# Performance work log

Measured on AMD Instinct MI355X. Metric: run time of the kernel, lower is better.

Reference implementation:

```python
import jax, jax.numpy as jnp
import numpy as np

B, S, D = 2, 2048, 2048
H, KVH = 32, 8
HD = D // H            # 64
G = H // KVH           # 4 kv groups
SCALE = 1.0 / np.sqrt(HD)


def setup_inputs() -> dict:
    key = jax.random.key(0)
    k1, k2, k3, k4, k5 = jax.random.split(key, 5)
    hidden_states = jax.random.normal(k1, (B, S, D), dtype=jnp.float32)
    Wq = jax.random.normal(k2, (D, H * HD), dtype=jnp.float32) * 0.02
    Wk = jax.random.normal(k3, (D, KVH * HD), dtype=jnp.float32) * 0.02
    Wv = jax.random.normal(k4, (D, KVH * HD), dtype=jnp.float32) * 0.02
    Wo = jax.random.normal(k5, (H * HD, D), dtype=jnp.float32) * 0.02
    return {"hidden_states": hidden_states, "Wq": Wq, "Wk": Wk, "Wv": Wv, "Wo": Wo}


def reference(hidden_states, Wq, Wk, Wv, Wo):
    B_, S_, _ = hidden_states.shape
    q = (hidden_states @ Wq).reshape(B_, S_, H, HD).transpose(0, 2, 1, 3)      # [B,H,S,HD]
    k = (hidden_states @ Wk).reshape(B_, S_, KVH, HD).transpose(0, 2, 1, 3)    # [B,KVH,S,HD]
    v = (hidden_states @ Wv).reshape(B_, S_, KVH, HD).transpose(0, 2, 1, 3)
    # repeat_interleave over head dim: kv head g serves q heads [g*G, (g+1)*G)
    k = jnp.repeat(k, G, axis=1)  # [B,H,S,HD]
    v = jnp.repeat(v, G, axis=1)
    scores = jnp.einsum('bhqd,bhkd->bhqk', q, k) * SCALE
    probs = jax.nn.softmax(scores.astype(jnp.float32), axis=-1).astype(q.dtype)
    # dropout is identity in eval mode
    out = jnp.einsum('bhqk,bhkd->bhqd', probs, v)             # [B,H,S,HD]
    out = out.transpose(0, 2, 1, 3).reshape(B_, S_, H * HD)   # [B,S,D]
    return out @ Wo
```

## Files before the change

### kernel.cpp

```cpp
#include <hip/hip_runtime.h>
#include <hip/hip_bf16.h>

typedef unsigned short u16;
typedef __attribute__((ext_vector_type(8))) short short8;
typedef __attribute__((ext_vector_type(4))) float f32x4;
typedef __attribute__((ext_vector_type(16))) float f32x16;
typedef __attribute__((ext_vector_type(4))) unsigned short u16x4;
typedef __attribute__((ext_vector_type(4))) int int4v;

#define S_LEN 2048
#define NH 32
#define NKV 8
#define QSCALE 0.18033688011112042f
#define PSHIFT 14.0f

__device__ __forceinline__ float fexp2(float x) { return __builtin_amdgcn_exp2f(x); }

__device__ __forceinline__ u16 f2bf(float f) {
  unsigned int u = __builtin_bit_cast(unsigned int, f);
  u += 0x7fffu + ((u >> 16) & 1u);
  return (u16)(u >> 16);
}

__device__ __forceinline__ unsigned int pk2bf(float a, float b) {
  float2 t; t.x = a; t.y = b;
  __hip_bfloat162 h = __float22bfloat162_rn(t);
  unsigned int r;
  __builtin_memcpy(&r, &h, 4);
  return r;
}

__device__ __forceinline__ void async16(const void* g, void* l) {
  __builtin_amdgcn_global_load_lds(
      (__attribute__((address_space(1))) void*)g,
      (__attribute__((address_space(3))) void*)l, 16, 0, 0);
}

__device__ __forceinline__ short8 mk_pf(unsigned a, unsigned b, unsigned c, unsigned d) {
  int4v t; t.x = (int)a; t.y = (int)b; t.z = (int)c; t.w = (int)d;
  return __builtin_bit_cast(short8, t);
}

__global__ __launch_bounds__(256) void prep_kernel(const float* __restrict__ X,
                                                   const float* __restrict__ Wq,
                                                   const float* __restrict__ Wk,
                                                   const float* __restrict__ Wv,
                                                   const float* __restrict__ Wo,
                                                   u16* __restrict__ Xb,
                                                   u16* __restrict__ Wqt,
                                                   u16* __restrict__ Wkt,
                                                   u16* __restrict__ Wvt,
                                                   u16* __restrict__ Wot) {
  __shared__ float tile[32][33];
  int bx = blockIdx.x, tid = threadIdx.x;
  if (bx < 8192) {
    int idx = bx * 256 + tid;
    float4 v = ((const float4*)X)[idx];
    u16x4 o;
    o.x = f2bf(v.x); o.y = f2bf(v.y); o.z = f2bf(v.z); o.w = f2bf(v.w);
    *(u16x4*)&Xb[(size_t)idx * 4] = o;
    return;
  }
  const float* in; u16* out; int N, bi;
  if (bx < 12288)      { bi = bx - 8192;  in = Wq; out = Wqt; N = 2048; }
  else if (bx < 13312) { bi = bx - 12288; in = Wk; out = Wkt; N = 512; }
  else if (bx < 14336) { bi = bx - 13312; in = Wv; out = Wvt; N = 512; }
  else                 { bi = bx - 14336; in = Wo; out = Wot; N = 2048; }
  const int K = 2048;
  int nbx = N >> 5;
  int n0 = (bi % nbx) * 32, k0 = (bi / nbx) * 32;
  int tx = tid & 31, ty = tid >> 5;
#pragma unroll
  for (int i = 0; i < 32; i += 8)
    tile[ty + i][tx] = in[(size_t)(k0 + ty + i) * N + n0 + tx];
  __syncthreads();
#pragma unroll
  for (int i = 0; i < 32; i += 8)
    out[(size_t)(n0 + ty + i) * K + k0 + tx] = f2bf(tile[tx][ty + i]);
}

__global__ __launch_bounds__(256) void gemm_qkv(const u16* __restrict__ A,
                                                const u16* __restrict__ Wqt,
                                                const u16* __restrict__ Wkvt,
                                                u16* __restrict__ Qb,
                                                u16* __restrict__ KVb) {
  __shared__ u16 lds_a[128 * 32];
  __shared__ u16 lds_b[128 * 32];
  int tid = threadIdx.x, bx = blockIdx.x;
  int mode, bm, bn;
  const u16* Bt;
  if (bx < 512) { mode = 0; bm = bx >> 4; bn = bx & 15; Bt = Wqt; }
  else          { mode = 1; int b2 = bx - 512; bm = b2 >> 3; bn = b2 & 7; Bt = Wkvt; }
  const int K = 2048;
  int w = tid >> 6, lane = tid & 63, qd = lane >> 4, ln = lane & 15;
  int wm = w >> 1, wn = w & 1;
  const f32x4 z4 = {0.f, 0.f, 0.f, 0.f};
  f32x4 acc[4][4];
#pragma unroll
  for (int i = 0; i < 4; ++i)
#pragma unroll
    for (int j = 0; j < 4; ++j) acc[i][j] = z4;

  const u16* Ab = A + (size_t)bm * 128 * K;
  const u16* Bb = Bt + (size_t)bn * 128 * K;
  int row0 = tid >> 2, c0 = tid & 3;
  int g0 = c0 ^ (row0 & 3) ^ ((row0 >> 2) & 3);
  int s1 = tid + 256, row1 = s1 >> 2, c1 = s1 & 3;
  int g1 = c1 ^ (row1 & 3) ^ ((row1 >> 2) & 3);
  int pat = (ln & 3) ^ ((ln >> 2) & 3);
  int goff = (qd ^ pat) * 8;

  for (int kt = 0; kt < K; kt += 32) {
    async16(Ab + (size_t)row0 * K + kt + g0 * 8, &lds_a[tid * 8]);
    async16(Ab + (size_t)row1 * K + kt + g1 * 8, &lds_a[2048 + tid * 8]);
    async16(Bb + (size_t)row0 * K + kt + g0 * 8, &lds_b[tid * 8]);
    async16(Bb + (size_t)row1 * K + kt + g1 * 8, &lds_b[2048 + tid * 8]);
    __syncthreads();
    short8 af[4], bf[4];
#pragma unroll
    for (int i = 0; i < 4; ++i)
      af[i] = *(const short8*)&lds_a[(wm * 64 + i * 16 + ln) * 32 + goff];
#pragma unroll
    for (int j = 0; j < 4; ++j)
      bf[j] = *(const short8*)&lds_b[(wn * 64 + j * 16 + ln) * 32 + goff];
#pragma unroll
    for (int i = 0; i < 4; ++i)
#pragma unroll
      for (int j = 0; j < 4; ++j)
        acc[i][j] = __builtin_amdgcn_mfma_f32_16x16x32_bf16(af[i], bf[j], acc[i][j], 0, 0, 0);
    __syncthreads();
  }

#pragma unroll
  for (int i = 0; i < 4; ++i)
#pragma unroll
    for (int r = 0; r < 4; ++r) {
      int m = bm * 128 + wm * 64 + i * 16 + qd * 4 + r;
      int b = m >> 11, s = m & 2047;
#pragma unroll
      for (int j = 0; j < 4; ++j) {
        int n = bn * 128 + wn * 64 + j * 16 + ln;
        float v = acc[i][j][r];
        int hh = n >> 6, hd = n & 63;
        if (mode == 0) {
          Qb[(((size_t)(b * NH + hh)) * S_LEN + s) * 64 + hd] = f2bf(v * QSCALE);
        } else {
          if (hh < 8)
            KVb[(((size_t)(b * NKV + hh)) * S_LEN + s) * 64 + hd] = f2bf(v);
          else
            KVb[2097152 + (((size_t)(b * NKV + (hh - 8))) * 64 + hd) * S_LEN + s] = f2bf(v);
        }
      }
    }
}

__global__ __launch_bounds__(256) void gemm_out(const u16* __restrict__ A,
                                                const u16* __restrict__ Bt,
                                                float* __restrict__ outp) {
  __shared__ u16 lds_a[128 * 32];
  __shared__ u16 lds_b[128 * 32];
  const int K = 2048, N = 2048;
  int tid = threadIdx.x;
  int bm = blockIdx.x >> 4, bn = blockIdx.x & 15;
  int w = tid >> 6, lane = tid & 63, qd = lane >> 4, ln = lane & 15;
  int wm = w >> 1, wn = w & 1;
  const f32x4 z4 = {0.f, 0.f, 0.f, 0.f};
  f32x4 acc[4][4];
#pragma unroll
  for (int i = 0; i < 4; ++i)
#pragma unroll
    for (int j = 0; j < 4; ++j) acc[i][j] = z4;

  const u16* Ab = A + (size_t)bm * 128 * K;
  const u16* Bb = Bt + (size_t)bn * 128 * K;
  int row0 = tid >> 2, c0 = tid & 3;
  int g0 = c0 ^ (row0 & 3) ^ ((row0 >> 2) & 3);
  int s1 = tid + 256, row1 = s1 >> 2, c1 = s1 & 3;
  int g1 = c1 ^ (row1 & 3) ^ ((row1 >> 2) & 3);
  int pat = (ln & 3) ^ ((ln >> 2) & 3);
  int goff = (qd ^ pat) * 8;

  for (int kt = 0; kt < K; kt += 32) {
    async16(Ab + (size_t)row0 * K + kt + g0 * 8, &lds_a[tid * 8]);
    async16(Ab + (size_t)row1 * K + kt + g1 * 8, &lds_a[2048 + tid * 8]);
    async16(Bb + (size_t)row0 * K + kt + g0 * 8, &lds_b[tid * 8]);
    async16(Bb + (size_t)row1 * K + kt + g1 * 8, &lds_b[2048 + tid * 8]);
    __syncthreads();
    short8 af[4], bf[4];
#pragma unroll
    for (int i = 0; i < 4; ++i)
      af[i] = *(const short8*)&lds_a[(wm * 64 + i * 16 + ln) * 32 + goff];
#pragma unroll
    for (int j = 0; j < 4; ++j)
      bf[j] = *(const short8*)&lds_b[(wn * 64 + j * 16 + ln) * 32 + goff];
#pragma unroll
    for (int i = 0; i < 4; ++i)
#pragma unroll
      for (int j = 0; j < 4; ++j)
        acc[i][j] = __builtin_amdgcn_mfma_f32_16x16x32_bf16(af[i], bf[j], acc[i][j], 0, 0, 0);
    __syncthreads();
  }

#pragma unroll
  for (int i = 0; i < 4; ++i)
#pragma unroll
    for (int r = 0; r < 4; ++r) {
      int m = bm * 128 + wm * 64 + i * 16 + qd * 4 + r;
#pragma unroll
      for (int j = 0; j < 4; ++j) {
        int n = bn * 128 + wn * 64 + j * 16 + ln;
        outp[(size_t)m * N + n] = acc[i][j][r];
      }
    }
}

__global__ __launch_bounds__(256) void attn_kernel(const u16* __restrict__ Q,
                                                   const u16* __restrict__ K,
                                                   const u16* __restrict__ VT,
                                                   u16* __restrict__ Ao) {
  __shared__ u16 lds_k[2][4096];
  __shared__ u16 lds_v[2][4096];
  int tid = threadIdx.x;
  int w = tid >> 6, lane = tid & 63;
  int l31 = lane & 31, l5 = lane >> 5;
  int qt = blockIdx.x & 15, bh = blockIdx.x >> 4;
  int b = bh >> 5, h = bh & 31, g = h >> 2;
  const u16* gQ = Q + ((size_t)bh * S_LEN + qt * 128) * 64;
  const u16* gK = K + (size_t)(b * NKV + g) * S_LEN * 64;
  const u16* gV = VT + (size_t)(b * NKV + g) * 64 * S_LEN;

  int p7 = l31 & 7;

  int s0 = tid, r0 = s0 >> 3, c0 = s0 & 7, gg0 = c0 ^ (r0 & 7);
  int s1 = tid + 256, r1 = s1 >> 3, c1 = s1 & 7, gg1 = c1 ^ (r1 & 7);

  u16* qstage = &lds_k[0][0];
#pragma unroll
  for (int k = 0; k < 4; ++k) {
    int s = tid + k * 256;
    int q = s >> 3, c = s & 7, gg = c ^ (q & 7);
    async16(gQ + (size_t)q * 64 + gg * 8, &qstage[s * 8]);
  }
  __syncthreads();
  short8 qf[4];
  int qrow = w * 32 + l31;
#pragma unroll
  for (int ks = 0; ks < 4; ++ks)
    qf[ks] = *(const short8*)&qstage[qrow * 64 + ((ks * 2 + l5) ^ p7) * 8];
  __syncthreads();

  async16(gK + (size_t)r0 * 64 + gg0 * 8, &lds_k[0][s0 * 8]);
  async16(gK + (size_t)r1 * 64 + gg1 * 8, &lds_k[0][s1 * 8]);
  async16(gV + (size_t)r0 * S_LEN + gg0 * 8, &lds_v[0][s0 * 8]);
  async16(gV + (size_t)r1 * S_LEN + gg1 * 8, &lds_v[0][s1 * 8]);

  const f32x16 psh16 = {-PSHIFT, -PSHIFT, -PSHIFT, -PSHIFT, -PSHIFT, -PSHIFT,
                        -PSHIFT, -PSHIFT, -PSHIFT, -PSHIFT, -PSHIFT, -PSHIFT,
                        -PSHIFT, -PSHIFT, -PSHIFT, -PSHIFT};
  f32x16 accO[2];
#pragma unroll
  for (int hb = 0; hb < 2; ++hb)
#pragma unroll
    for (int t = 0; t < 16; ++t) accO[hb][t] = 0.f;
  float li = 0.f;

  for (int c = 0; c < 32; ++c) {
    int cur = c & 1;
    if (c < 31) {
      int nb = cur ^ 1, cn = c + 1;
      async16(gK + (size_t)(cn * 64 + r0) * 64 + gg0 * 8, &lds_k[nb][s0 * 8]);
      async16(gK + (size_t)(cn * 64 + r1) * 64 + gg1 * 8, &lds_k[nb][s1 * 8]);
      async16(gV + (size_t)r0 * S_LEN + cn * 64 + gg0 * 8, &lds_v[nb][s0 * 8]);
      async16(gV + (size_t)r1 * S_LEN + cn * 64 + gg1 * 8, &lds_v[nb][s1 * 8]);
    }
    const u16* kb = lds_k[cur];
    const u16* vb = lds_v[cur];

#pragma unroll
    for (int kblk = 0; kblk < 2; ++kblk) {
      f32x16 sc = psh16;
      __builtin_amdgcn_s_setprio(1);
#pragma unroll
      for (int ks = 0; ks < 4; ++ks) {
        short8 kf = *(const short8*)&kb[(kblk * 32 + l31) * 64 + ((ks * 2 + l5) ^ p7) * 8];
        sc = __builtin_amdgcn_mfma_f32_32x32x16_bf16(kf, qf[ks], sc, 0, 0, 0);
      }
      __builtin_amdgcn_s_setprio(0);

      float p[16];
#pragma unroll
      for (int t = 0; t < 16; ++t) p[t] = fexp2(sc[t]);
#pragma unroll
      for (int t = 0; t < 16; t += 4) li += (p[t] + p[t + 1]) + (p[t + 2] + p[t + 3]);
      unsigned W[8];
#pragma unroll
      for (int t = 0; t < 8; ++t) W[t] = pk2bf(p[2 * t], p[2 * t + 1]);
      auto ra = __builtin_amdgcn_permlane32_swap((int)W[0], (int)W[2], false, false);
      auto rb = __builtin_amdgcn_permlane32_swap((int)W[1], (int)W[3], false, false);
      auto rc = __builtin_amdgcn_permlane32_swap((int)W[4], (int)W[6], false, false);
      auto rd = __builtin_amdgcn_permlane32_swap((int)W[5], (int)W[7], false, false);
      short8 pf0 = mk_pf((unsigned)ra[0], (unsigned)rb[0], (unsigned)ra[1], (unsigned)rb[1]);
      short8 pf1 = mk_pf((unsigned)rc[0], (unsigned)rd[0], (unsigned)rc[1], (unsigned)rd[1]);

      __builtin_amdgcn_s_setprio(1);
#pragma unroll
      for (int hb = 0; hb < 2; ++hb) {
        short8 vf = *(const short8*)&vb[(hb * 32 + l31) * 64 + ((kblk * 4 + l5) ^ p7) * 8];
        accO[hb] = __builtin_amdgcn_mfma_f32_32x32x16_bf16(vf, pf0, accO[hb], 0, 0, 0);
      }
#pragma unroll
      for (int hb = 0; hb < 2; ++hb) {
        short8 vf = *(const short8*)&vb[(hb * 32 + l31) * 64 + ((kblk * 4 + 2 + l5) ^ p7) * 8];
        accO[hb] = __builtin_amdgcn_mfma_f32_32x32x16_bf16(vf, pf1, accO[hb], 0, 0, 0);
      }
      __builtin_amdgcn_s_setprio(0);
    }
    __syncthreads();
  }

  float l = li + __shfl_xor(li, 32);
  float inv = 1.f / l;
  int q = qt * 128 + w * 32 + l31;
  size_t base = ((size_t)b * S_LEN + q) * 2048 + h * 64;
#pragma unroll
  for (int hb = 0; hb < 2; ++hb)
#pragma unroll
    for (int rq = 0; rq < 4; ++rq) {
      u16x4 o;
#pragma unroll
      for (int rr = 0; rr < 4; ++rr) o[rr] = f2bf(accO[hb][rq * 4 + rr] * inv);
      *(u16x4*)&Ao[base + hb * 32 + rq * 8 + l5 * 4] = o;
    }
}

extern "C" void kernel_launch(void* const* d_in, const int* in_sizes, int n_in,
                              void* d_out, int out_size, void* d_ws, size_t ws_size,
                              hipStream_t stream) {
  const float* X  = (const float*)d_in[0];
  const float* Wq = (const float*)d_in[1];
  const float* Wk = (const float*)d_in[2];
  const float* Wv = (const float*)d_in[3];
  const float* Wo = (const float*)d_in[4];
  char* ws = (char*)d_ws;
  u16* Xb  = (u16*)(ws);
  u16* Wqt = (u16*)(ws + 16777216);
  u16* Wkt = (u16*)(ws + 25165824);
  u16* Wvt = (u16*)(ws + 27262976);
  u16* Wot = (u16*)(ws + 29360128);
  u16* Qb  = (u16*)(ws + 37748736);
  u16* Kb  = (u16*)(ws + 54525952);
  u16* VTb = (u16*)(ws + 58720256);
  u16* Ab  = (u16*)(ws + 62914560);
  float* out = (float*)d_out;

  prep_kernel<<<18432, 256, 0, stream>>>(X, Wq, Wk, Wv, Wo, Xb, Wqt, Wkt, Wvt, Wot);
  gemm_qkv<<<768, 256, 0, stream>>>(Xb, Wqt, Wkt, Qb, Kb);
  attn_kernel<<<1024, 256, 0, stream>>>(Qb, Kb, VTb, Ab);
  gemm_out<<<512, 256, 0, stream>>>(Ab, Wot, out);
}
```

Baseline: 331.5 us.

## Double-buffer LDS tiles in QKV and output GEMMs with MFMA priority boost

Both projection GEMMs now use two LDS buffers per operand and prefetch the next K-slice with async copies while MFMAs run on the current slice. This is meant to hide global-load latency, which the old single-buffer loop exposed every iteration. s_setprio is raised around the MFMA block to favour matrix issue. LDS use doubles to 32KB per block, which may lower occupancy, and correctness depends on __syncthreads (which waits on vmcnt) ordering the async copies.

```diff
diff --git a/kernel.cpp b/kernel.cpp
--- a/kernel.cpp
+++ b/kernel.cpp
@@ -84,8 +84,7 @@
                                                 const u16* __restrict__ Wkvt,
                                                 u16* __restrict__ Qb,
                                                 u16* __restrict__ KVb) {
-  __shared__ u16 lds_a[128 * 32];
-  __shared__ u16 lds_b[128 * 32];
+  __shared__ u16 la0[4096], la1[4096], lb0[4096], lb1[4096];
   int tid = threadIdx.x, bx = blockIdx.x;
   int mode, bm, bn;
   const u16* Bt;
@@ -94,12 +93,11 @@
   const int K = 2048;
   int w = tid >> 6, lane = tid & 63, qd = lane >> 4, ln = lane & 15;
   int wm = w >> 1, wn = w & 1;
-  const f32x4 z4 = {0.f, 0.f, 0.f, 0.f};
   f32x4 acc[4][4];
 #pragma unroll
   for (int i = 0; i < 4; ++i)
 #pragma unroll
-    for (int j = 0; j < 4; ++j) acc[i][j] = z4;
+    for (int j = 0; j < 4; ++j) acc[i][j] = {0.f, 0.f, 0.f, 0.f};
 
   const u16* Ab = A + (size_t)bm * 128 * K;
   const u16* Bb = Bt + (size_t)bn * 128 * K;
@@ -109,27 +107,45 @@
   int g1 = c1 ^ (row1 & 3) ^ ((row1 >> 2) & 3);
   int pat = (ln & 3) ^ ((ln >> 2) & 3);
   int goff = (qd ^ pat) * 8;
-
-  for (int kt = 0; kt < K; kt += 32) {
-    async16(Ab + (size_t)row0 * K + kt + g0 * 8, &lds_a[tid * 8]);
-    async16(Ab + (size_t)row1 * K + kt + g1 * 8, &lds_a[2048 + tid * 8]);
-    async16(Bb + (size_t)row0 * K + kt + g0 * 8, &lds_b[tid * 8]);
-    async16(Bb + (size_t)row1 * K + kt + g1 * 8, &lds_b[2048 + tid * 8]);
-    __syncthreads();
-    short8 af[4], bf[4];
-#pragma unroll
-    for (int i = 0; i < 4; ++i)
-      af[i] = *(const short8*)&lds_a[(wm * 64 + i * 16 + ln) * 32 + goff];
-#pragma unroll
-    for (int j = 0; j < 4; ++j)
-      bf[j] = *(const short8*)&lds_b[(wn * 64 + j * 16 + ln) * 32 + goff];
-#pragma unroll
-    for (int i = 0; i < 4; ++i)
-#pragma unroll
-      for (int j = 0; j < 4; ++j)
-        acc[i][j] = __builtin_amdgcn_mfma_f32_16x16x32_bf16(af[i], bf[j], acc[i][j], 0, 0, 0);
-    __syncthreads();
-  }
+  const u16* pa0 = Ab + (size_t)row0 * K + g0 * 8;
+  const u16* pa1 = Ab + (size_t)row1 * K + g1 * 8;
+  const u16* pb0 = Bb + (size_t)row0 * K + g0 * 8;
+  const u16* pb1 = Bb + (size_t)row1 * K + g1 * 8;
+
+#define QKV_STAGE(LA, LB, OFS)                      \
+  async16(pa0 + (OFS), &LA[tid * 8]);               \
+  async16(pa1 + (OFS), &LA[2048 + tid * 8]);        \
+  async16(pb0 + (OFS), &LB[tid * 8]);               \
+  async16(pb1 + (OFS), &LB[2048 + tid * 8]);
+
+#define QKV_COMPUTE(LA, LB)                                                        \
+  {                                                                                \
+    short8 af[4], bf[4];                                                           \
+    _Pragma("unroll") for (int i = 0; i < 4; ++i)                                  \
+        af[i] = *(const short8*)&LA[(wm * 64 + i * 16 + ln) * 32 + goff];          \
+    _Pragma("unroll") for (int j = 0; j < 4; ++j)                                  \
+        bf[j] = *(const short8*)&LB[(wn * 64 + j * 16 + ln) * 32 + goff];          \
+    __builtin_amdgcn_s_setprio(1);                                                 \
+    _Pragma("unroll") for (int i = 0; i < 4; ++i)                                  \
+      _Pragma("unroll") for (int j = 0; j < 4; ++j)                                \
+        acc[i][j] =                                                                \
+            __builtin_amdgcn_mfma_f32_16x16x32_bf16(af[i], bf[j], acc[i][j], 0, 0, 0); \
+    __builtin_amdgcn_s_setprio(0);                                                 \
+  }
+
+  QKV_STAGE(la0, lb0, 0);
+  __syncthreads();
+
+  for (int kt = 0; kt < K; kt += 64) {
+    QKV_STAGE(la1, lb1, kt + 32);
+    QKV_COMPUTE(la0, lb0);
+    __syncthreads();
+    if (kt + 64 < K) { QKV_STAGE(la0, lb0, kt + 64); }
+    QKV_COMPUTE(la1, lb1);
+    __syncthreads();
+  }
+#undef QKV_STAGE
+#undef QKV_COMPUTE
 
 #pragma unroll
   for (int i = 0; i < 4; ++i)
@@ -157,19 +173,17 @@
 __global__ __launch_bounds__(256) void gemm_out(const u16* __restrict__ A,
                                                 const u16* __restrict__ Bt,
                                                 float* __restrict__ outp) {
-  __shared__ u16 lds_a[128 * 32];
-  __shared__ u16 lds_b[128 * 32];
+  __shared__ u16 la0[4096], la1[4096], lb0[4096], lb1[4096];
   const int K = 2048, N = 2048;
   int tid = threadIdx.x;
   int bm = blockIdx.x >> 4, bn = blockIdx.x & 15;
   int w = tid >> 6, lane = tid & 63, qd = lane >> 4, ln = lane & 15;
   int wm = w >> 1, wn = w & 1;
-  const f32x4 z4 = {0.f, 0.f, 0.f, 0.f};
   f32x4 acc[4][4];
 #pragma unroll
   for (int i = 0; i < 4; ++i)
 #pragma unroll
-    for (int j = 0; j < 4; ++j) acc[i][j] = z4;
+    for (int j = 0; j < 4; ++j) acc[i][j] = {0.f, 0.f, 0.f, 0.f};
 
   const u16* Ab = A + (size_t)bm * 128 * K;
   const u16* Bb = Bt + (size_t)bn * 128 * K;
@@ -179,27 +193,45 @@
   int g1 = c1 ^ (row1 & 3) ^ ((row1 >> 2) & 3);
   int pat = (ln & 3) ^ ((ln >> 2) & 3);
   int goff = (qd ^ pat) * 8;
-
-  for (int kt = 0; kt < K; kt += 32) {
-    async16(Ab + (size_t)row0 * K + kt + g0 * 8, &lds_a[tid * 8]);
-    async16(Ab + (size_t)row1 * K + kt + g1 * 8, &lds_a[2048 + tid * 8]);
-    async16(Bb + (size_t)row0 * K + kt + g0 * 8, &lds_b[tid * 8]);
-    async16(Bb + (size_t)row1 * K + kt + g1 * 8, &lds_b[2048 + tid * 8]);
-    __syncthreads();
-    short8 af[4], bf[4];
-#pragma unroll
-    for (int i = 0; i < 4; ++i)
-      af[i] = *(const short8*)&lds_a[(wm * 64 + i * 16 + ln) * 32 + goff];
-#pragma unroll
-    for (int j = 0; j < 4; ++j)
-      bf[j] = *(const short8*)&lds_b[(wn * 64 + j * 16 + ln) * 32 + goff];
-#pragma unroll
-    for (int i = 0; i < 4; ++i)
-#pragma unroll
-      for (int j = 0; j < 4; ++j)
-        acc[i][j] = __builtin_amdgcn_mfma_f32_16x16x32_bf16(af[i], bf[j], acc[i][j], 0, 0, 0);
-    __syncthreads();
-  }
+  const u16* pa0 = Ab + (size_t)row0 * K + g0 * 8;
+  const u16* pa1 = Ab + (size_t)row1 * K + g1 * 8;
+  const u16* pb0 = Bb + (size_t)row0 * K + g0 * 8;
+  const u16* pb1 = Bb + (size_t)row1 * K + g1 * 8;
+
+#define OUT_STAGE(LA, LB, OFS)                      \
+  async16(pa0 + (OFS), &LA[tid * 8]);               \
+  async16(pa1 + (OFS), &LA[2048 + tid * 8]);        \
+  async16(pb0 + (OFS), &LB[tid * 8]);               \
+  async16(pb1 + (OFS), &LB[2048 + tid * 8]);
+
+#define OUT_COMPUTE(LA, LB)                                                        \
+  {                                                                                \
+    short8 af[4], bf[4];                                                           \
+    _Pragma("unroll") for (int i = 0; i < 4; ++i)                                  \
+        af[i] = *(const short8*)&LA[(wm * 64 + i * 16 + ln) * 32 + goff];          \
+    _Pragma("unroll") for (int j = 0; j < 4; ++j)                                  \
+        bf[j] = *(const short8*)&LB[(wn * 64 + j * 16 + ln) * 32 + goff];          \
+    __builtin_amdgcn_s_setprio(1);                                                 \
+    _Pragma("unroll") for (int i = 0; i < 4; ++i)                                  \
+      _Pragma("unroll") for (int j = 0; j < 4; ++j)                                \
+        acc[i][j] =                                                                \
+            __builtin_amdgcn_mfma_f32_16x16x32_bf16(af[i], bf[j], acc[i][j], 0, 0, 0); \
+    __builtin_amdgcn_s_setprio(0);                                                 \
+  }
+
+  OUT_STAGE(la0, lb0, 0);
+  __syncthreads();
+
+  for (int kt = 0; kt < K; kt += 64) {
+    OUT_STAGE(la1, lb1, kt + 32);
+    OUT_COMPUTE(la0, lb0);
+    __syncthreads();
+    if (kt + 64 < K) { OUT_STAGE(la0, lb0, kt + 64); }
+    OUT_COMPUTE(la1, lb1);
+    __syncthreads();
+  }
+#undef OUT_STAGE
+#undef OUT_COMPUTE
 
 #pragma unroll
   for (int i = 0; i < 4; ++i)
```

New measurement: 324.1 us. 1.02x faster.
